# Performance work log

Measured on AMD Instinct MI355X. Metric: run time of the kernel, lower is better.

The kernel has to match this reference:

```python
import jax, jax.numpy as jnp
import numpy as np

KERNEL_MUL = 2.0
KERNEL_NUM = 5

def setup_inputs() -> dict:
    key = jax.random.key(0)
    k1, k2 = jax.random.split(key)
    source = jax.random.normal(k1, (4096, 256), dtype=jnp.float32)
    target = jax.random.normal(k2, (4096, 256), dtype=jnp.float32)
    return {"source": source, "target": target}

def reference(source, target):
    B = source.shape[0]
    total = jnp.concatenate([source, target], axis=0)           # [2N, D]
    n = total.shape[0]
    # pairwise squared L2 distances via expansion (same math as
    # ((total0 - total1)**2).sum(2) without the [2N,2N,D] intermediate)
    sq = jnp.sum(total * total, axis=-1)                         # [2N]
    l2 = jnp.maximum(sq[:, None] + sq[None, :] - 2.0 * (total @ total.T), 0.0)  # [2N,2N]
    # bandwidth from data mean of off-diagonal distances (detached in torch via .data)
    bandwidth = jax.lax.stop_gradient(jnp.sum(l2)) / (n * n - n)
    bandwidth = bandwidth / (KERNEL_MUL ** (KERNEL_NUM // 2))
    kernels = jnp.zeros_like(l2)
    for i in range(KERNEL_NUM):
        kernels = kernels + jnp.exp(-l2 / (bandwidth * (KERNEL_MUL ** i)))
    xx = kernels[:B, :B]
    yy = kernels[B:, B:]
    xy = kernels[:B, B:]
    yx = kernels[B:, :B]
    return jnp.mean(xx + yy - xy - yx)
```

## Files before the change

kernel.cpp:

```cpp
#include <hip/hip_runtime.h>


#define NROWS 8192
#define BHALF 4096
#define DDIM  256
#define TILE  128
#define NTILE 64
#define NBLK  2080

typedef __attribute__((ext_vector_type(8))) short bf16x8;
typedef __attribute__((ext_vector_type(4))) float f32x4;
typedef __attribute__((ext_vector_type(4))) unsigned short u16x4;

struct Ws {
  float Ssum;
  float colsum[256];
  float coef;
  float sq[NROWS];
  float part[NBLK];
};

__device__ __forceinline__ unsigned short f2bf(float x) {
  unsigned int u = __builtin_bit_cast(unsigned int, x);
  return (unsigned short)((u + 0x7fffu + ((u >> 16) & 1u)) >> 16);
}

__device__ __forceinline__ const float* row_ptr(const float* src, const float* tgt, int i) {
  return (i < BHALF) ? (src + (size_t)i * DDIM) : (tgt + (size_t)(i - BHALF) * DDIM);
}

__global__ __launch_bounds__(256) void k_prep(const float* __restrict__ src,
                                              const float* __restrict__ tgt,
                                              Ws* __restrict__ ws,
                                              unsigned short* __restrict__ tb,
                                              int conv) {
  __shared__ float cls[4][256];
  int tid = threadIdx.x, wave = tid >> 6, lane = tid & 63;
  int row0 = blockIdx.x * 32 + wave * 8;
  float c0 = 0.f, c1 = 0.f, c2 = 0.f, c3 = 0.f;
  float s[8];
  #pragma unroll
  for (int r = 0; r < 8; ++r) {
    const float4* rp = (const float4*)row_ptr(src, tgt, row0 + r);
    float4 x = rp[lane];
    if (conv) {
      u16x4 b = { f2bf(x.x), f2bf(x.y), f2bf(x.z), f2bf(x.w) };
      *(u16x4*)&tb[(size_t)(row0 + r) * DDIM + lane * 4] = b;
    }
    c0 += x.x; c1 += x.y; c2 += x.z; c3 += x.w;
    s[r] = x.x * x.x + x.y * x.y + x.z * x.z + x.w * x.w;
  }
  #pragma unroll
  for (int off = 32; off > 0; off >>= 1) {
    #pragma unroll
    for (int r = 0; r < 8; ++r) s[r] += __shfl_xor(s[r], off);
  }
  if (lane == 0) {
    float Sw = 0.f;
    #pragma unroll
    for (int r = 0; r < 8; ++r) { ws->sq[row0 + r] = s[r]; Sw += s[r]; }
    atomicAdd(&ws->Ssum, Sw);
  }
  cls[wave][lane * 4 + 0] = c0;
  cls[wave][lane * 4 + 1] = c1;
  cls[wave][lane * 4 + 2] = c2;
  cls[wave][lane * 4 + 3] = c3;
  __syncthreads();
  atomicAdd(&ws->colsum[tid], cls[0][tid] + cls[1][tid] + cls[2][tid] + cls[3][tid]);
}

__global__ __launch_bounds__(256) void k_bw(Ws* __restrict__ ws) {
  __shared__ float red[4];
  int tid = threadIdx.x, wave = tid >> 6, lane = tid & 63;
  float mc = ws->colsum[tid];
  float p = mc * mc;
  #pragma unroll
  for (int off = 32; off > 0; off >>= 1) p += __shfl_xor(p, off);
  if (lane == 0) red[wave] = p;
  __syncthreads();
  if (tid == 0) {
    float msq = red[0] + red[1] + red[2] + red[3];
    float S = ws->Ssum;
    double n = (double)NROWS;
    double sum_l2 = 2.0 * n * (double)S - 2.0 * (double)msq;
    double bw = sum_l2 / (n * n - n) / 4.0;
    ws->coef = (float)(1.4426950408889634 / (16.0 * bw));
  }
}

__device__ __forceinline__ void stage_tiles(const unsigned short* gA,
                                            const unsigned short* gB,
                                            unsigned short* lA, unsigned short* lB,
                                            int kc) {
  #pragma unroll
  for (int t = 0; t < 4; ++t) {
    __builtin_amdgcn_global_load_lds(
        (const __attribute__((address_space(1))) void*)(gA + (size_t)(t * 8) * DDIM + kc * 64),
        (__attribute__((address_space(3))) void*)(lA + (t * 8) * 64), 16, 0, 0);
    __builtin_amdgcn_global_load_lds(
        (const __attribute__((address_space(1))) void*)(gB + (size_t)(t * 8) * DDIM + kc * 64),
        (__attribute__((address_space(3))) void*)(lB + (t * 8) * 64), 16, 0, 0);
  }
}

template <int FAST>
__global__ __launch_bounds__(256) void k_main(const unsigned short* __restrict__ tb,
                                              const float* __restrict__ src,
                                              const float* __restrict__ tgt,
                                              Ws* __restrict__ ws) {
  int idx = blockIdx.x;
  int ti = (int)((129.0 - sqrt(129.0 * 129.0 - 8.0 * (double)idx)) * 0.5);
  while (64 * (ti + 1) - ((ti + 1) * ti) / 2 <= idx) ++ti;
  while (64 * ti - (ti * (ti - 1)) / 2 > idx) --ti;
  int tj = ti + (idx - (64 * ti - (ti * (ti - 1)) / 2));

  __shared__ __align__(16) unsigned short As[2][TILE * 64];
  __shared__ __align__(16) unsigned short Bs[2][TILE * 64];
  __shared__ float wsum[4];

  int tid = threadIdx.x;
  int wave = tid >> 6, lane = tid & 63;
  int wm = wave >> 1, wn = wave & 1;
  int lr = lane & 15, q = lane >> 4;
  int Ib = ti * TILE, Jb = tj * TILE;

  float coef = ws->coef;
  float coef2 = 2.f * coef;
  int ibase = Ib + wm * 64;
  int jbase = Jb + wn * 64;
  float scj[4], sci[16];
  #pragma unroll
  for (int n = 0; n < 4; ++n) scj[n] = ws->sq[jbase + n * 16 + lr] * coef;
  #pragma unroll
  for (int m = 0; m < 4; ++m)
    #pragma unroll
    for (int r = 0; r < 4; ++r)
      sci[m * 4 + r] = ws->sq[ibase + m * 16 + q * 4 + r] * coef;

  f32x4 zero = {0.f, 0.f, 0.f, 0.f};
  f32x4 acc[4][4];
  #pragma unroll
  for (int m = 0; m < 4; ++m)
    #pragma unroll
    for (int n = 0; n < 4; ++n) acc[m][n] = zero;

  const unsigned short* gA = nullptr; const unsigned short* gB = nullptr;
  if (FAST) {
    int lrow = lane >> 3;
    int lchk = (lane & 7) ^ lrow;
    gA = tb + (size_t)(Ib + wave * 32 + lrow) * DDIM + lchk * 8;
    gB = tb + (size_t)(Jb + wave * 32 + lrow) * DDIM + lchk * 8;
  }
  int r0 = tid >> 4, c4 = tid & 15;

  if (FAST) stage_tiles(gA, gB, &As[0][(wave * 32) * 64], &Bs[0][(wave * 32) * 64], 0);
  else {
    #pragma unroll
    for (int rr = 0; rr < 8; ++rr) {
      int row = rr * 16 + r0;
      int sw = ((c4 >> 1) ^ (row & 7)) * 8 + (c4 & 1) * 4;
      float4 va = ((const float4*)row_ptr(src, tgt, Ib + row))[c4];
      u16x4 ba = { f2bf(va.x), f2bf(va.y), f2bf(va.z), f2bf(va.w) };
      *(u16x4*)&As[0][row * 64 + sw] = ba;
      float4 vb = ((const float4*)row_ptr(src, tgt, Jb + row))[c4];
      u16x4 bb = { f2bf(vb.x), f2bf(vb.y), f2bf(vb.z), f2bf(vb.w) };
      *(u16x4*)&Bs[0][row * 64 + sw] = bb;
    }
  }

  #pragma unroll
  for (int kc = 0; kc < 4; ++kc) {
    __syncthreads();
    int nxt = (kc + 1) & 1;
    if (kc < 3) {
      if (FAST) stage_tiles(gA, gB, &As[nxt][(wave * 32) * 64], &Bs[nxt][(wave * 32) * 64], kc + 1);
      else {
        #pragma unroll
        for (int rr = 0; rr < 8; ++rr) {
          int row = rr * 16 + r0;
          int sw = ((c4 >> 1) ^ (row & 7)) * 8 + (c4 & 1) * 4;
          float4 va = ((const float4*)row_ptr(src, tgt, Ib + row))[(kc + 1) * 16 + c4];
          u16x4 ba = { f2bf(va.x), f2bf(va.y), f2bf(va.z), f2bf(va.w) };
          *(u16x4*)&As[nxt][row * 64 + sw] = ba;
          float4 vb = ((const float4*)row_ptr(src, tgt, Jb + row))[(kc + 1) * 16 + c4];
          u16x4 bb = { f2bf(vb.x), f2bf(vb.y), f2bf(vb.z), f2bf(vb.w) };
          *(u16x4*)&Bs[nxt][row * 64 + sw] = bb;
        }
      }
    }
    int cur = kc & 1;
    const unsigned short* lA = &As[cur][0];
    const unsigned short* lB = &Bs[cur][0];
    #pragma unroll
    for (int kk = 0; kk < 2; ++kk) {
      int cidx = ((kk * 4 + q) ^ (lr & 7)) << 3;
      bf16x8 af[4], bfr[4];
      #pragma unroll
      for (int m = 0; m < 4; ++m)
        af[m] = *(const bf16x8*)&lA[(wm * 64 + m * 16 + lr) * 64 + cidx];
      #pragma unroll
      for (int n = 0; n < 4; ++n)
        bfr[n] = *(const bf16x8*)&lB[(wn * 64 + n * 16 + lr) * 64 + cidx];
      #pragma unroll
      for (int m = 0; m < 4; ++m)
        #pragma unroll
        for (int n = 0; n < 4; ++n)
          acc[m][n] = __builtin_amdgcn_mfma_f32_16x16x32_bf16(af[m], bfr[n], acc[m][n], 0, 0, 0);
    }
  }

  float lsum = 0.f;
  #pragma unroll
  for (int m = 0; m < 4; ++m) {
    #pragma unroll
    for (int n = 0; n < 4; ++n) {
      f32x4 g = acc[m][n];
      #pragma unroll
      for (int r = 0; r < 4; ++r) {
        float arg = fminf(coef2 * g[r] - sci[m * 4 + r] - scj[n], 0.f);
        float t  = __builtin_amdgcn_exp2f(arg);
        float t2 = t * t, t4 = t2 * t2, t8 = t4 * t4, t16 = t8 * t8;
        lsum += ((t + t2) + (t4 + t8)) + t16;
      }
    }
  }
  #pragma unroll
  for (int off = 32; off > 0; off >>= 1) lsum += __shfl_xor(lsum, off);
  if (lane == 0) wsum[wave] = lsum;
  __syncthreads();
  if (tid == 0) {
    float tot = wsum[0] + wsum[1] + wsum[2] + wsum[3];
    float sA = (ti < 32) ? 1.f : -1.f;
    float sB = (tj < 32) ? 1.f : -1.f;
    float fac = sA * sB * ((ti == tj) ? 1.f : 2.f);
    ws->part[blockIdx.x] = fac * tot;
  }
}

__global__ __launch_bounds__(256) void k_final(const Ws* __restrict__ ws,
                                               float* __restrict__ out) {
  __shared__ double red[4];
  int tid = threadIdx.x, wave = tid >> 6, lane = tid & 63;
  double s = 0.0;
  for (int i = tid; i < NBLK; i += 256) s += (double)ws->part[i];
  #pragma unroll
  for (int off = 32; off > 0; off >>= 1) s += __shfl_xor(s, off);
  if (lane == 0) red[wave] = s;
  __syncthreads();
  if (tid == 0)
    out[0] = (float)((red[0] + red[1] + red[2] + red[3]) /
                     ((double)BHALF * (double)BHALF));
}

extern "C" void kernel_launch(void* const* d_in, const int* in_sizes, int n_in,
                              void* d_out, int out_size, void* d_ws, size_t ws_size,
                              hipStream_t stream) {
  const float* src = (const float*)d_in[0];
  const float* tgt = (const float*)d_in[1];
  Ws* ws = (Ws*)d_ws;
  float* out = (float*)d_out;

  size_t wsoff = (sizeof(Ws) + 255) & ~(size_t)255;
  size_t need = wsoff + (size_t)NROWS * DDIM * 2;
  bool fast = ws_size >= need;
  unsigned short* tb = fast ? (unsigned short*)((char*)d_ws + wsoff) : nullptr;

  hipMemsetAsync(d_ws, 0, 1056, stream);
  hipLaunchKernelGGL(k_prep, dim3(256), dim3(256), 0, stream, src, tgt, ws, tb,
                     fast ? 1 : 0);
  hipLaunchKernelGGL(k_bw, dim3(1), dim3(256), 0, stream, ws);
  if (fast)
    hipLaunchKernelGGL((k_main<1>), dim3(NBLK), dim3(256), 0, stream, tb, src, tgt, ws);
  else
    hipLaunchKernelGGL((k_main<0>), dim3(NBLK), dim3(256), 0, stream, tb, src, tgt, ws);
  hipLaunchKernelGGL(k_final, dim3(1), dim3(256), 0, stream, ws, out);
}
```

Before: 121.8 us.

## Single-buffer LDS, packed-float epilogue, and atomic-free prep reductions

```diff
diff --git a/kernel.cpp b/kernel.cpp
--- a/kernel.cpp
+++ b/kernel.cpp
@@ -10,12 +10,13 @@
 
 typedef __attribute__((ext_vector_type(8))) short bf16x8;
 typedef __attribute__((ext_vector_type(4))) float f32x4;
+typedef __attribute__((ext_vector_type(2))) float f32x2;
 typedef __attribute__((ext_vector_type(4))) unsigned short u16x4;
 
 struct Ws {
-  float Ssum;
-  float colsum[256];
   float coef;
+  float Spart[256];
+  float cpart[256][256];
   float sq[NROWS];
   float part[NBLK];
 };
@@ -35,6 +36,7 @@
                                               unsigned short* __restrict__ tb,
                                               int conv) {
   __shared__ float cls[4][256];
+  __shared__ float sred[4];
   int tid = threadIdx.x, wave = tid >> 6, lane = tid & 63;
   int row0 = blockIdx.x * 32 + wave * 8;
   float c0 = 0.f, c1 = 0.f, c2 = 0.f, c3 = 0.f;
@@ -59,28 +61,34 @@
     float Sw = 0.f;
     #pragma unroll
     for (int r = 0; r < 8; ++r) { ws->sq[row0 + r] = s[r]; Sw += s[r]; }
-    atomicAdd(&ws->Ssum, Sw);
+    sred[wave] = Sw;
   }
   cls[wave][lane * 4 + 0] = c0;
   cls[wave][lane * 4 + 1] = c1;
   cls[wave][lane * 4 + 2] = c2;
   cls[wave][lane * 4 + 3] = c3;
   __syncthreads();
-  atomicAdd(&ws->colsum[tid], cls[0][tid] + cls[1][tid] + cls[2][tid] + cls[3][tid]);
+  ws->cpart[blockIdx.x][tid] = cls[0][tid] + cls[1][tid] + cls[2][tid] + cls[3][tid];
+  if (tid == 0) ws->Spart[blockIdx.x] = sred[0] + sred[1] + sred[2] + sred[3];
 }
 
 __global__ __launch_bounds__(256) void k_bw(Ws* __restrict__ ws) {
-  __shared__ float red[4];
+  __shared__ float redm[4], reds[4];
   int tid = threadIdx.x, wave = tid >> 6, lane = tid & 63;
-  float mc = ws->colsum[tid];
+  float mc = 0.f;
+  for (int b = 0; b < 256; ++b) mc += ws->cpart[b][tid];
   float p = mc * mc;
-  #pragma unroll
-  for (int off = 32; off > 0; off >>= 1) p += __shfl_xor(p, off);
-  if (lane == 0) red[wave] = p;
+  float sp = ws->Spart[tid];
+  #pragma unroll
+  for (int off = 32; off > 0; off >>= 1) {
+    p  += __shfl_xor(p, off);
+    sp += __shfl_xor(sp, off);
+  }
+  if (lane == 0) { redm[wave] = p; reds[wave] = sp; }
   __syncthreads();
   if (tid == 0) {
-    float msq = red[0] + red[1] + red[2] + red[3];
-    float S = ws->Ssum;
+    float msq = redm[0] + redm[1] + redm[2] + redm[3];
+    float S   = reds[0] + reds[1] + reds[2] + reds[3];
     double n = (double)NROWS;
     double sum_l2 = 2.0 * n * (double)S - 2.0 * (double)msq;
     double bw = sum_l2 / (n * n - n) / 4.0;
@@ -104,18 +112,18 @@
 }
 
 template <int FAST>
-__global__ __launch_bounds__(256) void k_main(const unsigned short* __restrict__ tb,
-                                              const float* __restrict__ src,
-                                              const float* __restrict__ tgt,
-                                              Ws* __restrict__ ws) {
+__global__ __launch_bounds__(256, 4) void k_main(const unsigned short* __restrict__ tb,
+                                                 const float* __restrict__ src,
+                                                 const float* __restrict__ tgt,
+                                                 Ws* __restrict__ ws) {
   int idx = blockIdx.x;
   int ti = (int)((129.0 - sqrt(129.0 * 129.0 - 8.0 * (double)idx)) * 0.5);
   while (64 * (ti + 1) - ((ti + 1) * ti) / 2 <= idx) ++ti;
   while (64 * ti - (ti * (ti - 1)) / 2 > idx) --ti;
   int tj = ti + (idx - (64 * ti - (ti * (ti - 1)) / 2));
 
-  __shared__ __align__(16) unsigned short As[2][TILE * 64];
-  __shared__ __align__(16) unsigned short Bs[2][TILE * 64];
+  __shared__ __align__(16) unsigned short As[TILE * 64];
+  __shared__ __align__(16) unsigned short Bs[TILE * 64];
   __shared__ float wsum[4];
 
   int tid = threadIdx.x;
@@ -128,14 +136,17 @@
   float coef2 = 2.f * coef;
   int ibase = Ib + wm * 64;
   int jbase = Jb + wn * 64;
-  float scj[4], sci[16];
-  #pragma unroll
-  for (int n = 0; n < 4; ++n) scj[n] = ws->sq[jbase + n * 16 + lr] * coef;
-  #pragma unroll
-  for (int m = 0; m < 4; ++m)
-    #pragma unroll
-    for (int r = 0; r < 4; ++r)
-      sci[m * 4 + r] = ws->sq[ibase + m * 16 + q * 4 + r] * coef;
+  float nscj[4];
+  f32x2 nsci01[4], nsci23[4];
+  #pragma unroll
+  for (int n = 0; n < 4; ++n) nscj[n] = -ws->sq[jbase + n * 16 + lr] * coef;
+  #pragma unroll
+  for (int m = 0; m < 4; ++m) {
+    nsci01[m] = f32x2{ -ws->sq[ibase + m * 16 + q * 4 + 0] * coef,
+                       -ws->sq[ibase + m * 16 + q * 4 + 1] * coef };
+    nsci23[m] = f32x2{ -ws->sq[ibase + m * 16 + q * 4 + 2] * coef,
+                       -ws->sq[ibase + m * 16 + q * 4 + 3] * coef };
+  }
 
   f32x4 zero = {0.f, 0.f, 0.f, 0.f};
   f32x4 acc[4][4];
@@ -153,54 +164,35 @@
   }
   int r0 = tid >> 4, c4 = tid & 15;
 
-  if (FAST) stage_tiles(gA, gB, &As[0][(wave * 32) * 64], &Bs[0][(wave * 32) * 64], 0);
-  else {
-    #pragma unroll
-    for (int rr = 0; rr < 8; ++rr) {
-      int row = rr * 16 + r0;
-      int sw = ((c4 >> 1) ^ (row & 7)) * 8 + (c4 & 1) * 4;
-      float4 va = ((const float4*)row_ptr(src, tgt, Ib + row))[c4];
-      u16x4 ba = { f2bf(va.x), f2bf(va.y), f2bf(va.z), f2bf(va.w) };
-      *(u16x4*)&As[0][row * 64 + sw] = ba;
-      float4 vb = ((const float4*)row_ptr(src, tgt, Jb + row))[c4];
-      u16x4 bb = { f2bf(vb.x), f2bf(vb.y), f2bf(vb.z), f2bf(vb.w) };
-      *(u16x4*)&Bs[0][row * 64 + sw] = bb;
-    }
-  }
-
   #pragma unroll
   for (int kc = 0; kc < 4; ++kc) {
+    if (kc) __syncthreads();
+    if (FAST) {
+      stage_tiles(gA, gB, &As[(wave * 32) * 64], &Bs[(wave * 32) * 64], kc);
+    } else {
+      #pragma unroll
+      for (int rr = 0; rr < 8; ++rr) {
+        int row = rr * 16 + r0;
+        int sw = ((c4 >> 1) ^ (row & 7)) * 8 + (c4 & 1) * 4;
+        float4 va = ((const float4*)row_ptr(src, tgt, Ib + row))[kc * 16 + c4];
+        u16x4 ba = { f2bf(va.x), f2bf(va.y), f2bf(va.z), f2bf(va.w) };
+        *(u16x4*)&As[row * 64 + sw] = ba;
+        float4 vb = ((const float4*)row_ptr(src, tgt, Jb + row))[kc * 16 + c4];
+        u16x4 bb = { f2bf(vb.x), f2bf(vb.y), f2bf(vb.z), f2bf(vb.w) };
+        *(u16x4*)&Bs[row * 64 + sw] = bb;
+      }
+    }
     __syncthreads();
-    int nxt = (kc + 1) & 1;
-    if (kc < 3) {
-      if (FAST) stage_tiles(gA, gB, &As[nxt][(wave * 32) * 64], &Bs[nxt][(wave * 32) * 64], kc + 1);
-      else {
-        #pragma unroll
-        for (int rr = 0; rr < 8; ++rr) {
-          int row = rr * 16 + r0;
-          int sw = ((c4 >> 1) ^ (row & 7)) * 8 + (c4 & 1) * 4;
-          float4 va = ((const float4*)row_ptr(src, tgt, Ib + row))[(kc + 1) * 16 + c4];
-          u16x4 ba = { f2bf(va.x), f2bf(va.y), f2bf(va.z), f2bf(va.w) };
-          *(u16x4*)&As[nxt][row * 64 + sw] = ba;
-          float4 vb = ((const float4*)row_ptr(src, tgt, Jb + row))[(kc + 1) * 16 + c4];
-          u16x4 bb = { f2bf(vb.x), f2bf(vb.y), f2bf(vb.z), f2bf(vb.w) };
-          *(u16x4*)&Bs[nxt][row * 64 + sw] = bb;
-        }
-      }
-    }
-    int cur = kc & 1;
-    const unsigned short* lA = &As[cur][0];
-    const unsigned short* lB = &Bs[cur][0];
     #pragma unroll
     for (int kk = 0; kk < 2; ++kk) {
       int cidx = ((kk * 4 + q) ^ (lr & 7)) << 3;
       bf16x8 af[4], bfr[4];
       #pragma unroll
       for (int m = 0; m < 4; ++m)
-        af[m] = *(const bf16x8*)&lA[(wm * 64 + m * 16 + lr) * 64 + cidx];
+        af[m] = *(const bf16x8*)&As[(wm * 64 + m * 16 + lr) * 64 + cidx];
       #pragma unroll
       for (int n = 0; n < 4; ++n)
-        bfr[n] = *(const bf16x8*)&lB[(wn * 64 + n * 16 + lr) * 64 + cidx];
+        bfr[n] = *(const bf16x8*)&Bs[(wn * 64 + n * 16 + lr) * 64 + cidx];
       #pragma unroll
       for (int m = 0; m < 4; ++m)
         #pragma unroll
@@ -209,21 +201,35 @@
     }
   }
 
-  float lsum = 0.f;
+  const f32x2 c2v = { coef2, coef2 };
+  f32x2 accA = {0.f, 0.f}, accB = {0.f, 0.f};
+  f32x2 accC = {0.f, 0.f}, accD = {0.f, 0.f};
   #pragma unroll
   for (int m = 0; m < 4; ++m) {
     #pragma unroll
     for (int n = 0; n < 4; ++n) {
       f32x4 g = acc[m][n];
-      #pragma unroll
-      for (int r = 0; r < 4; ++r) {
-        float arg = fminf(coef2 * g[r] - sci[m * 4 + r] - scj[n], 0.f);
-        float t  = __builtin_amdgcn_exp2f(arg);
-        float t2 = t * t, t4 = t2 * t2, t8 = t4 * t4, t16 = t8 * t8;
-        lsum += ((t + t2) + (t4 + t8)) + t16;
-      }
-    }
-  }
+      f32x2 bj = { nscj[n], nscj[n] };
+      f32x2 b01 = nsci01[m] + bj;
+      f32x2 b23 = nsci23[m] + bj;
+      f32x2 a01 = f32x2{g[0], g[1]} * c2v + b01;
+      f32x2 a23 = f32x2{g[2], g[3]} * c2v + b23;
+      f32x2 t0, t1;
+      t0.x = __builtin_amdgcn_exp2f(a01.x); t0.y = __builtin_amdgcn_exp2f(a01.y);
+      t1.x = __builtin_amdgcn_exp2f(a23.x); t1.y = __builtin_amdgcn_exp2f(a23.y);
+      f32x2 p0 = t0 * t0, p1 = t1 * t1;
+      f32x2 q0 = p0 * p0, q1 = p1 * p1;
+      f32x2 r0v = q0 * q0, r1v = q1 * q1;
+      accA += t0 + p0;
+      accB += q0 + r0v;
+      accA = r0v * r0v + accA;
+      accC += t1 + p1;
+      accD += q1 + r1v;
+      accC = r1v * r1v + accC;
+    }
+  }
+  float lsum = (accA.x + accA.y) + (accB.x + accB.y)
+             + (accC.x + accC.y) + (accD.x + accD.y);
   #pragma unroll
   for (int off = 32; off > 0; off >>= 1) lsum += __shfl_xor(lsum, off);
   if (lane == 0) wsum[wave] = lsum;
@@ -265,7 +271,6 @@
   bool fast = ws_size >= need;
   unsigned short* tb = fast ? (unsigned short*)((char*)d_ws + wsoff) : nullptr;
 
-  hipMemsetAsync(d_ws, 0, 1056, stream);
   hipLaunchKernelGGL(k_prep, dim3(256), dim3(256), 0, stream, src, tgt, ws, tb,
                      fast ? 1 : 0);
   hipLaunchKernelGGL(k_bw, dim3(1), dim3(256), 0, stream, ws);
```

Measured after the change: 107.3 us. -11.9%, faster.
